# Optimization experiments

Hardware: AMD Instinct MI355X
Metric: run time of the kernel (lower is better)

The kernel has to match this reference:

```python
import jax, jax.numpy as jnp
import numpy as np

IN_CHN, OUT_CHN, K = 64, 64, 3
STRIDE, PADDING = 1, 1


def setup_inputs() -> dict:
    key = jax.random.key(0)
    k1, k2 = jax.random.split(key)
    Activation = jax.random.normal(k1, (32, IN_CHN, 112, 112), dtype=jnp.float32)
    weights = jax.random.uniform(k2, (IN_CHN * OUT_CHN * K * K, 1), dtype=jnp.float32) * 0.001
    return {"Activation": Activation, "weights": weights}


def _binarize_ste(x):
    # sign(x) in forward, identity gradient (straight-through estimator)
    return x + jax.lax.stop_gradient(jnp.sign(x) - x)


def reference(Activation, weights):
    real_weights = weights.reshape(OUT_CHN, IN_CHN, K, K)
    bin_act = _binarize_ste(Activation)      # [N, C, H, W], values in {-1, 0, 1}
    bin_w = _binarize_ste(real_weights)      # [O, I, K, K]
    out = jax.lax.conv_general_dilated(
        bin_act, bin_w,
        window_strides=(STRIDE, STRIDE),
        padding=[(PADDING, PADDING), (PADDING, PADDING)],
        dimension_numbers=("NCHW", "OIHW", "NCHW"),
    )
    return out
```

## Files before the change

kernel.cpp:

```cpp
#include <hip/hip_runtime.h>
#include <stdint.h>


#define NN 32
#define CC 64
#define HH 112
#define WW 112
#define OO 64
#define HW (HH*WW)
#define NHW (NN*HW)

#define PACK_BLOCK 256
#define PIXG 4
#define PACK_A_THREADS (NHW/PIXG)
#define PACK_A_BLOCKS (PACK_A_THREADS/PACK_BLOCK)

#define CONV_BLOCK 256
#define CONV_BLOCKS (NHW/CONV_BLOCK)

__global__ __launch_bounds__(PACK_BLOCK)
void pack_kernel(const float* __restrict__ act, const float* __restrict__ wgt,
                 uint64_t* __restrict__ ap, uint64_t* __restrict__ wp) {
    int b = blockIdx.x;
    if (b == PACK_A_BLOCKS) {
        for (int t = threadIdx.x; t < OO * 9; t += PACK_BLOCK) {
            int o = t / 9, k = t - o * 9;
            uint32_t lo = 0, hi = 0;
            #pragma unroll
            for (int i = 0; i < 64; ++i) {
                uint32_t s = __float_as_uint(wgt[(o * 64 + i) * 9 + k]) >> 31;
                if (i < 32) lo |= s << i;
                else        hi |= s << (i - 32);
            }
            wp[t] = ((uint64_t)hi << 32) | lo;
        }
        return;
    }
    int t = b * PACK_BLOCK + threadIdx.x;
    int n = t / (HW / 4);
    int rem4 = t - n * (HW / 4);
    const float4* base = (const float4*)act + (size_t)n * CC * (HW / 4) + rem4;
    uint32_t lo[4] = {0, 0, 0, 0}, hi[4] = {0, 0, 0, 0};
    #pragma unroll
    for (int c = 0; c < 64; ++c) {
        float4 v = base[(size_t)c * (HW / 4)];
        uint32_t s0 = __float_as_uint(v.x) >> 31;
        uint32_t s1 = __float_as_uint(v.y) >> 31;
        uint32_t s2 = __float_as_uint(v.z) >> 31;
        uint32_t s3 = __float_as_uint(v.w) >> 31;
        if (c < 32) {
            lo[0] |= s0 << c; lo[1] |= s1 << c; lo[2] |= s2 << c; lo[3] |= s3 << c;
        } else {
            int cc = c - 32;
            hi[0] |= s0 << cc; hi[1] |= s1 << cc; hi[2] |= s2 << cc; hi[3] |= s3 << cc;
        }
    }
    ulonglong2 w01, w23;
    w01.x = ((uint64_t)hi[0] << 32) | lo[0];
    w01.y = ((uint64_t)hi[1] << 32) | lo[1];
    w23.x = ((uint64_t)hi[2] << 32) | lo[2];
    w23.y = ((uint64_t)hi[3] << 32) | lo[3];
    ulonglong2* dst = (ulonglong2*)(ap + (size_t)t * 4);
    dst[0] = w01;
    dst[1] = w23;
}

__global__ __launch_bounds__(CONV_BLOCK)
void conv_kernel(const uint64_t* __restrict__ ap, const uint64_t* __restrict__ wp,
                 float* __restrict__ out) {
    int idx = blockIdx.x * CONV_BLOCK + threadIdx.x;
    int n = idx / HW;
    int rem = idx - n * HW;
    int h = rem / WW;
    int w = rem - h * WW;
    const uint64_t* apn = ap + (size_t)n * HW;

    uint64_t a[9], m[9];
    int nvalid = 0;
    #pragma unroll
    for (int kh = 0; kh < 3; ++kh) {
        int hh = h + kh - 1;
        bool hv = (unsigned)hh < (unsigned)HH;
        #pragma unroll
        for (int kw = 0; kw < 3; ++kw) {
            int ww2 = w + kw - 1;
            bool wv = (unsigned)ww2 < (unsigned)WW;
            bool v = hv && wv;
            int k = kh * 3 + kw;
            int ch = hv ? hh : h;
            int cw = wv ? ww2 : w;
            a[k] = apn[ch * WW + cw];
            m[k] = v ? ~0ull : 0ull;
            nvalid += v ? 1 : 0;
        }
    }
    int base = 64 * nvalid;
    float* op = out + (size_t)n * (OO * HW) + rem;
    for (int o = 0; o < OO; ++o) {
        const uint64_t* wk = wp + o * 9;
        int s = 0;
        #pragma unroll
        for (int k = 0; k < 9; ++k)
            s += __popcll((a[k] ^ wk[k]) & m[k]);
        op[(size_t)o * HW] = (float)(base - 2 * s);
    }
}

extern "C" void kernel_launch(void* const* d_in, const int* in_sizes, int n_in,
                              void* d_out, int out_size, void* d_ws, size_t ws_size,
                              hipStream_t stream) {
    const float* act = (const float*)d_in[0];
    const float* wgt = (const float*)d_in[1];
    float* out = (float*)d_out;

    uint64_t* wp = (uint64_t*)d_ws;
    uint64_t* ap = wp + 1024;

    pack_kernel<<<PACK_A_BLOCKS + 1, PACK_BLOCK, 0, stream>>>(act, wgt, ap, wp);
    conv_kernel<<<CONV_BLOCKS, CONV_BLOCK, 0, stream>>>(ap, wp, out);
}
```

Measured before the change: 209.1 us.

## Split conv into interior two-pixel threads and masked border threads

The conv kernel now has two block types. Interior pixels are handled two per thread, with 12 loaded activation words shared across two outputs, no validity masks and float2 stores. Border pixels (top and bottom rows plus two columns on each side) keep the masked per-pixel path. This removes mask work and halves the weight loads per output in the interior, at the cost of more indexing complexity and halving the interior thread count.

```diff
diff --git a/kernel.cpp b/kernel.cpp
--- a/kernel.cpp
+++ b/kernel.cpp
@@ -11,12 +11,19 @@
 #define NHW (NN*HW)
 
 #define PACK_BLOCK 256
-#define PIXG 4
-#define PACK_A_THREADS (NHW/PIXG)
-#define PACK_A_BLOCKS (PACK_A_THREADS/PACK_BLOCK)
+#define PACK_A_BLOCKS (NHW/4/PACK_BLOCK)
 
-#define CONV_BLOCK 256
-#define CONV_BLOCKS (NHW/CONV_BLOCK)
+#define INT_GPR 54
+#define INT_ROWS 110
+#define INT_GPI (INT_GPR*INT_ROWS)
+#define INT_THREADS (NN*INT_GPI)
+#define INT_BLOCKS ((INT_THREADS+255)/256)
+
+#define BOR_PPI 664
+#define BOR_THREADS (NN*BOR_PPI)
+#define BOR_BLOCKS (BOR_THREADS/256)
+
+#define CONV_BLOCKS (BOR_BLOCKS + INT_BLOCKS)
 
 __global__ __launch_bounds__(PACK_BLOCK)
 void pack_kernel(const float* __restrict__ act, const float* __restrict__ wgt,
@@ -65,16 +72,55 @@
     dst[1] = w23;
 }
 
-__global__ __launch_bounds__(CONV_BLOCK)
+__global__ __launch_bounds__(256)
 void conv_kernel(const uint64_t* __restrict__ ap, const uint64_t* __restrict__ wp,
                  float* __restrict__ out) {
-    int idx = blockIdx.x * CONV_BLOCK + threadIdx.x;
-    int n = idx / HW;
-    int rem = idx - n * HW;
-    int h = rem / WW;
-    int w = rem - h * WW;
+    if (blockIdx.x >= BOR_BLOCKS) {
+        int t = (blockIdx.x - BOR_BLOCKS) * 256 + threadIdx.x;
+        if (t >= INT_THREADS) return;
+        int n = t / INT_GPI;
+        int rem = t - n * INT_GPI;
+        int hr = rem / INT_GPR;
+        int gw = rem - hr * INT_GPR;
+        int h = hr + 1;
+        int w0 = 2 + 2 * gw;
+        const uint64_t* apn = ap + (size_t)n * HW + (h - 1) * WW + (w0 - 1);
+        uint64_t a[3][4];
+        #pragma unroll
+        for (int r = 0; r < 3; ++r)
+            #pragma unroll
+            for (int c = 0; c < 4; ++c)
+                a[r][c] = apn[r * WW + c];
+        float* op = out + (size_t)n * (OO * HW) + h * WW + w0;
+        for (int o = 0; o < OO; ++o) {
+            const uint64_t* wk = wp + o * 9;
+            int s0 = 0, s1 = 0;
+            #pragma unroll
+            for (int r = 0; r < 3; ++r)
+                #pragma unroll
+                for (int c = 0; c < 3; ++c) {
+                    uint64_t w = wk[r * 3 + c];
+                    s0 += __popcll(a[r][c]     ^ w);
+                    s1 += __popcll(a[r][c + 1] ^ w);
+                }
+            float2 v = make_float2((float)(576 - 2 * s0), (float)(576 - 2 * s1));
+            *(float2*)(op + (size_t)o * HW) = v;
+        }
+        return;
+    }
+    int t = blockIdx.x * 256 + threadIdx.x;
+    int n = t / BOR_PPI;
+    int b = t - n * BOR_PPI;
+    int h, w;
+    if (b < 112)      { h = 0;   w = b; }
+    else if (b < 224) { h = 111; w = b - 112; }
+    else {
+        int c = b - 224;
+        h = 1 + (c >> 2);
+        int q = c & 3;
+        w = q + ((q >= 2) ? 108 : 0);
+    }
     const uint64_t* apn = ap + (size_t)n * HW;
-
     uint64_t a[9], m[9];
     int nvalid = 0;
     #pragma unroll
@@ -95,7 +141,7 @@
         }
     }
     int base = 64 * nvalid;
-    float* op = out + (size_t)n * (OO * HW) + rem;
+    float* op = out + (size_t)n * (OO * HW) + h * WW + w;
     for (int o = 0; o < OO; ++o) {
         const uint64_t* wk = wp + o * 9;
         int s = 0;
@@ -117,5 +163,5 @@
     uint64_t* ap = wp + 1024;
 
     pack_kernel<<<PACK_A_BLOCKS + 1, PACK_BLOCK, 0, stream>>>(act, wgt, ap, wp);
-    conv_kernel<<<CONV_BLOCKS, CONV_BLOCK, 0, stream>>>(ap, wp, out);
+    conv_kernel<<<CONV_BLOCKS, 256, 0, stream>>>(ap, wp, out);
 }
```

Measured after the change: 233.1 us. 1.11x slower.
